# Kernel tuning notes

Measured on AMD Instinct MI355X. Metric: run time of the kernel, lower is better.

Reference implementation:

```python
import jax, jax.numpy as jnp
import numpy as np

B, T, D = 2, 2048, 1024
K, F = 8, 4096
LAMBDA = 0.5


def setup_inputs() -> dict:
    key = jax.random.key(0)
    ks = jax.random.split(key, 8)
    s = 0.02
    return {
        "x": jax.random.normal(ks[0], (B, T, D), dtype=jnp.float32),
        "prev_logits": jax.random.normal(ks[1], (B, T, K), dtype=jnp.float32),
        "Wt": jax.random.normal(ks[2], (D, K), dtype=jnp.float32) * s,
        "Wgt": jax.random.normal(ks[3], (K, K), dtype=jnp.float32) * s,
        "We_logits": jnp.zeros((K,), dtype=jnp.float32),
        "W1": jax.random.normal(ks[4], (K, D, F), dtype=jnp.float32) * s,
        "b1": jnp.zeros((K, F), dtype=jnp.float32),
        "W2": jax.random.normal(ks[5], (K, F, D), dtype=jnp.float32) * s,
        "b2": jnp.zeros((K, D), dtype=jnp.float32),
    }


def reference(x, prev_logits, Wt, Wgt, We_logits, W1, b1, W2, b2):
    # gating: softmax over router logits, sigmoid-threshold multi-hot mask
    logits = jnp.einsum("btd,dk->btk", x, Wt) + jnp.einsum("btk,kj->btj", prev_logits, Wgt)
    st = jax.nn.softmax(logits, axis=-1)                       # (B,T,K)
    We = jax.nn.sigmoid(We_logits)                             # (K,)
    mask = (st > LAMBDA * We).astype(x.dtype)                  # (B,T,K)
    g = st * mask
    sel_counts = mask.sum(axis=(0, 1))                         # (K,)
    avg_density = mask.sum(axis=-1).mean()                     # scalar

    # dense multi-expert FFN: every expert on every token (dropout=0 / eval)
    h = jax.nn.gelu(jnp.einsum("btd,kdf->bktf", x, W1) + b1[:, None, :], approximate=False)
    outk = jnp.einsum("bktf,kfd->bktd", h, W2) + b2[:, None, :]  # (B,K,T,D)
    y = jnp.einsum("btk,bktd->btd", g, outk)
    y = y / (g.sum(axis=-1, keepdims=True) + 1e-6)
    return y, jax.lax.stop_gradient(logits), sel_counts, avg_density
```

## Files before the change

kernel.cpp:

```cpp
#include <hip/hip_runtime.h>
#include <cstdint>
#include <cstddef>

#define NB 2
#define NTT 2048
#define ND 1024
#define NK 8
#define NF 4096
#define NTOK (NB*NTT)
#define LAMBDA_C 0.5f

#define Y_SZ   (NTOK*ND)
#define LG_OFF Y_SZ
#define SC_OFF (LG_OFF + NTOK*NK)
#define AD_OFF (SC_OFF + NK)

#define WS_CNT    0
#define WS_SEG    8
#define WS_NTILES 17
#define WS_TILEK  32
#define WS_TILER  1056
#define WS_PTOK   4096
#define WS_PCOEF  36864
#define WS_COEF   69632
#define WS_X16    102400
#define WS_H      2199552

#define BM 128
#define BN 128
#define BK 64
#define SPLITK2 4
#define KT 16

#define ASL0 0u
#define ASL1 16384u
#define BSL0 32768u
#define BSL1 49152u

typedef float  f32x4  __attribute__((ext_vector_type(4)));
typedef float  f32x16 __attribute__((ext_vector_type(16)));
typedef _Float16 f16x8 __attribute__((ext_vector_type(8)));
typedef unsigned int u32x4 __attribute__((ext_vector_type(4)));

__device__ __forceinline__ unsigned int pkrtz(float a, float b){
    auto h = __builtin_amdgcn_cvt_pkrtz(a, b);
    return __builtin_bit_cast(unsigned int, h);
}
__device__ __forceinline__ float gelu_exact(float v){
    return 0.5f * v * (1.0f + erff(v * 0.70710678118654752440f));
}

__global__ __launch_bounds__(256) void k_xcast(const float* __restrict__ x,
                                               unsigned short* __restrict__ x16)
{
    int i = (blockIdx.x*256 + threadIdx.x) * 16;
    const f32x4* src = (const f32x4*)(x + i);
    f32x4 v0 = src[0], v1 = src[1], v2 = src[2], v3 = src[3];
    u32x4 o0 = {pkrtz(v0[0],v0[1]), pkrtz(v0[2],v0[3]), pkrtz(v1[0],v1[1]), pkrtz(v1[2],v1[3])};
    u32x4 o1 = {pkrtz(v2[0],v2[1]), pkrtz(v2[2],v2[3]), pkrtz(v3[0],v3[1]), pkrtz(v3[2],v3[3])};
    *(u32x4*)(x16 + i)     = o0;
    *(u32x4*)(x16 + i + 8) = o1;
}

__global__ __launch_bounds__(256) void k_gating(
    const float* __restrict__ x, const float* __restrict__ pl,
    const float* __restrict__ Wt, const float* __restrict__ Wgt,
    const float* __restrict__ Wel, float* __restrict__ out,
    float* __restrict__ coef, int* __restrict__ cnt)
{
    int t = blockIdx.x;
    const float* xt = x + (size_t)t * ND;
    float acc[NK] = {0,0,0,0,0,0,0,0};
    for (int d = threadIdx.x; d < ND; d += 256){
        float xv = xt[d];
        const float4* w = (const float4*)(Wt + (size_t)d * NK);
        float4 w0 = w[0], w1 = w[1];
        acc[0] += xv*w0.x; acc[1] += xv*w0.y; acc[2] += xv*w0.z; acc[3] += xv*w0.w;
        acc[4] += xv*w1.x; acc[5] += xv*w1.y; acc[6] += xv*w1.z; acc[7] += xv*w1.w;
    }
    __shared__ float red[4][NK];
    #pragma unroll
    for (int k = 0; k < NK; k++){
        float v = acc[k];
        #pragma unroll
        for (int off = 32; off; off >>= 1) v += __shfl_down(v, off);
        if ((threadIdx.x & 63) == 0) red[threadIdx.x >> 6][k] = v;
    }
    __syncthreads();
    if (threadIdx.x == 0){
        const float* p = pl + (size_t)t * NK;
        float pv[NK];
        #pragma unroll
        for (int j = 0; j < NK; j++) pv[j] = p[j];
        float lg[NK]; float mx = -1e30f;
        #pragma unroll
        for (int k = 0; k < NK; k++){
            float v = red[0][k] + red[1][k] + red[2][k] + red[3][k];
            #pragma unroll
            for (int j = 0; j < NK; j++) v += pv[j] * Wgt[j*NK + k];
            lg[k] = v; mx = fmaxf(mx, v);
            out[LG_OFF + (size_t)t*NK + k] = v;
        }
        float e[NK]; float s = 0.f;
        #pragma unroll
        for (int k = 0; k < NK; k++){ e[k] = expf(lg[k] - mx); s += e[k]; }
        float g[NK]; float gsum = 0.f;
        #pragma unroll
        for (int k = 0; k < NK; k++){
            float st = e[k] / s;
            float we = 1.f / (1.f + expf(-Wel[k]));
            bool m = st > LAMBDA_C * we;
            g[k] = m ? st : 0.f;
            gsum += g[k];
        }
        float inv = 1.f / (gsum + 1e-6f);
        #pragma unroll
        for (int k = 0; k < NK; k++){
            coef[(size_t)t*NK + k] = g[k] * inv;
            if (g[k] > 0.f) atomicAdd(&cnt[k], 1);
        }
    }
}

__global__ __launch_bounds__(256) void k_scan(
    const float* __restrict__ coef, int* __restrict__ wsi,
    float* __restrict__ wsf, int pair_cap)
{
    int k = blockIdx.x;
    const int* cnt = wsi + WS_CNT;
    int base = 0;
    for (int j = 0; j < k; j++) base += cnt[j];
    int tid = threadIdx.x, lane = tid & 63, w = tid >> 6;
    __shared__ int wsum[4];
    __shared__ int sbase;
    if (tid == 0){
        sbase = base;
        wsi[WS_SEG + k] = base;
        if (k == NK-1) wsi[WS_SEG + NK] = base + cnt[k];
    }
    __syncthreads();
    int* ptok = wsi + WS_PTOK;
    float* pc = wsf + WS_PCOEF;
    for (int c0 = 0; c0 < NTOK; c0 += 256){
        int t = c0 + tid;
        float c = coef[(size_t)t*NK + k];
        bool m = c > 0.f;
        unsigned long long bal = __ballot(m);
        int pre = __popcll(bal & ((1ull << lane) - 1ull));
        if (lane == 0) wsum[w] = __popcll(bal);
        __syncthreads();
        int b = sbase;
        for (int j = 0; j < w; j++) b += wsum[j];
        if (m){
            int pos = b + pre;
            if (pos < pair_cap){ ptok[pos] = t; pc[pos] = c; }
        }
        __syncthreads();
        if (tid == 0) sbase += wsum[0] + wsum[1] + wsum[2] + wsum[3];
        __syncthreads();
    }
}

__global__ void k_tiles(int* __restrict__ wsi, float* __restrict__ out, int pair_cap)
{
    if (threadIdx.x == 0 && blockIdx.x == 0){
        const int* cnt = wsi + WS_CNT;
        const int* seg = wsi + WS_SEG;
        int total = 0;
        for (int k = 0; k < NK; k++){ total += cnt[k]; out[SC_OFF + k] = (float)cnt[k]; }
        out[AD_OFF] = (float)total / (float)NTOK;
        int nt = 0;
        for (int k = 0; k < NK; k++){
            int e = min(seg[k+1], pair_cap);
            for (int r = seg[k]; r < e; r += BM){
                wsi[WS_TILEK + nt] = k; wsi[WS_TILER + nt] = r; nt++;
            }
        }
        wsi[WS_NTILES] = nt;
    }
}

#define XCD_PART_LOOP(nwork)                                              \
    int q_ = (nwork) >> 3, rr_ = (nwork) & 7;                             \
    int xcd_ = blockIdx.x & 7;                                            \
    int slot_ = blockIdx.x >> 3;                                          \
    int nslot_ = gridDim.x >> 3;                                          \
    int cntw_ = q_ + (xcd_ < rr_ ? 1 : 0);                                \
    int start_ = xcd_ * q_ + (xcd_ < rr_ ? xcd_ : rr_);                   \
    for (int p_ = slot_; p_ < cntw_; p_ += nslot_)


#define LOADB(tt_, LDW_)                                                  \
  { const float* bn_ = bsrc + (size_t)((tt_)*BK + bu*8)*(LDW_);           \
    _Pragma("unroll")                                                     \
    for (int r9_ = 0; r9_ < 8; r9_++) gb[r9_] = *(const f32x4*)(bn_ + (size_t)r9_*(LDW_)); }

#define CVTWRB(BO_)                                                       \
  { _Pragma("unroll")                                                     \
    for (int j9_ = 0; j9_ < 4; j9_++){                                    \
        unsigned p0_ = pkrtz(gb[0][j9_], gb[1][j9_]);                     \
        unsigned p1_ = pkrtz(gb[2][j9_], gb[3][j9_]);                     \
        unsigned p2_ = pkrtz(gb[4][j9_], gb[5][j9_]);                     \
        unsigned p3_ = pkrtz(gb[6][j9_], gb[7][j9_]);                     \
        unsigned c9_ = (unsigned)(bg*4 + j9_);                            \
        unsigned off9_ = (BO_) + c9_*128u + (((unsigned)bu*16u) ^ (((c9_>>1)&7u)<<4)); \
        *(u32x4*)(&lds[off9_]) = (u32x4){p0_, p1_, p2_, p3_};             \
    } }

#define GLL_A(AO_, tt_)                                                   \
  { _Pragma("unroll")                                                     \
    for (int c9_ = 0; c9_ < 4; c9_++){                                    \
        const unsigned short* g9_ = asrc[c9_] + (tt_)*BK + asw8;          \
        __builtin_amdgcn_global_load_lds(                                 \
            (const __attribute__((address_space(1))) void*)g9_,           \
            (__attribute__((address_space(3))) void*)(&lds[(AO_) + (unsigned)((wv*4 + c9_)*1024)]), \
            16, 0, 0);                                                    \
    } }

#define MFMA_PH(AO_, BO_)                                                 \
  { __builtin_amdgcn_s_setprio(1);                                        \
    _Pragma("unroll")                                                     \
    for (int s9_ = 0; s9_ < 4; s9_++){                                    \
        unsigned ko_ = (unsigned)(s9_*32) + ah16;                         \
        f16x8 a0_ = *(const f16x8*)(&lds[(AO_) + arow0*128u + (ko_ ^ axr)]); \
        f16x8 a1_ = *(const f16x8*)(&lds[(AO_) + arow1*128u + (ko_ ^ axr)]); \
        f16x8 b0_ = *(const f16x8*)(&lds[(BO_) + bcol0*128u + (ko_ ^ bxr)]); \
        f16x8 b1_ = *(const f16x8*)(&lds[(BO_) + bcol1*128u + (ko_ ^ bxr)]); \
        acc00 = __builtin_amdgcn_mfma_f32_32x32x16_f16(a0_, b0_, acc00, 0,0,0); \
        acc01 = __builtin_amdgcn_mfma_f32_32x32x16_f16(a0_, b1_, acc01, 0,0,0); \
        acc10 = __builtin_amdgcn_mfma_f32_32x32x16_f16(a1_, b0_, acc10, 0,0,0); \
        acc11 = __builtin_amdgcn_mfma_f32_32x32x16_f16(a1_, b1_, acc11, 0,0,0); \
    }                                                                     \
    __builtin_amdgcn_s_setprio(0); }

#define PIPE_LOOP(LDW_)                                                   \
    f32x16 acc00 = {0}, acc01 = {0}, acc10 = {0}, acc11 = {0};            \
    LOADB(0, LDW_)                                                        \
    GLL_A(ASL0, 0)                                                        \
    for (int t = 0; t < KT-1; t++){                                       \
        if ((t & 1) == 0){                                                \
            CVTWRB(BSL0)                                                  \
            LOADB(t+1, LDW_)                                              \
            asm volatile("s_waitcnt vmcnt(8) lgkmcnt(0)" ::: "memory");   \
            __builtin_amdgcn_s_barrier();                                 \
            __builtin_amdgcn_sched_barrier(0);                            \
            GLL_A(ASL1, t+1)                                              \
            MFMA_PH(ASL0, BSL0)                                           \
        } else {                                                          \
            CVTWRB(BSL1)                                                  \
            LOADB(t+1, LDW_)                                              \
            asm volatile("s_waitcnt vmcnt(8) lgkmcnt(0)" ::: "memory");   \
            __builtin_amdgcn_s_barrier();                                 \
            __builtin_amdgcn_sched_barrier(0);                            \
            GLL_A(ASL0, t+1)                                              \
            MFMA_PH(ASL1, BSL1)                                           \
        }                                                                 \
    }                                                                     \
    {                                     \
        CVTWRB(BSL1)                                                      \
        asm volatile("s_waitcnt vmcnt(0) lgkmcnt(0)" ::: "memory");       \
        __builtin_amdgcn_s_barrier();                                     \
        __builtin_amdgcn_sched_barrier(0);                                \
        MFMA_PH(ASL1, BSL1)                                               \
    }

__global__ __launch_bounds__(256, 2) void k_gemm1(
    const unsigned short* __restrict__ x16, const float* __restrict__ W1,
    const float* __restrict__ b1, const int* __restrict__ wsi,
    unsigned short* __restrict__ hbuf, int pair_cap)
{
    __shared__ char lds[65536];
    __shared__ int stok[BM];
    const int* seg  = wsi + WS_SEG;
    const int* tk   = wsi + WS_TILEK;
    const int* tr   = wsi + WS_TILER;
    const int* ptok = wsi + WS_PTOK;
    int ntm = wsi[WS_NTILES];
    int nwork = ntm * (NF / BN);
    int tid  = threadIdx.x;
    int L    = tid & 63;
    int wv   = tid >> 6;
    int wr = wv >> 1, wc = wv & 1;
    int bu = tid >> 5, bg = tid & 31;
    unsigned l31 = (unsigned)(L & 31);
    unsigned arow0 = (unsigned)(wr*64) + l31;
    unsigned arow1 = arow0 + 32u;
    unsigned bcol0 = BSL0*0 + (unsigned)(wc*64) + l31;
    unsigned bcol1 = bcol0 + 32u;
    unsigned ah16 = (unsigned)((L >> 5) * 16);
    unsigned axr  = (unsigned)((L & 7) << 4);
    unsigned bxr  = ((l31 >> 1) & 7u) << 4;
    int asw8 = ((L & 7) ^ (L >> 3)) * 8;
    int srow = L >> 3;

    XCD_PART_LOOP(nwork){
        int widx = start_ + p_;
        int mt = widx % ntm;
        int ft = widx / ntm;
        int kexp = tk[mt];
        int row0 = tr[mt];
        int nrows = min(BM, seg[kexp+1] - row0);
        int f0 = ft * BN;
        __syncthreads();
        if (tid < BM){
            int r = row0 + tid;
            stok[tid] = (tid < nrows && r < pair_cap) ? ptok[r] : ptok[row0];
        }
        __syncthreads();
        const unsigned short* asrc[4];
        #pragma unroll
        for (int c = 0; c < 4; c++)
            asrc[c] = x16 + (size_t)stok[(wv*4 + c)*8 + srow] * ND;
        const float* bsrc = W1 + (size_t)kexp*ND*NF + f0 + bg*4;
        f32x4 gb[8];
        PIPE_LOOP(NF)
        const float* b1k = b1 + (size_t)kexp*NF;
        #pragma unroll
        for (int n = 0; n < 2; n++){
            int f = f0 + wc*64 + n*32 + (int)l31;
            float bv = b1k[f];
            #pragma unroll
            for (int m = 0; m < 2; m++){
                int rbase = wr*64 + m*32 + 4*(L>>5);
                const f32x16& a = (m==0) ? (n==0 ? acc00 : acc01) : (n==0 ? acc10 : acc11);
                #pragma unroll
                for (int rg = 0; rg < 16; rg++){
                    int row = rbase + (rg&3) + 8*(rg>>2);
                    if (row < nrows && row0 + row < pair_cap){
                        float v = gelu_exact(a[rg] + bv);
                        hbuf[(size_t)(row0+row)*NF + f] = (unsigned short)(pkrtz(v, 0.f) & 0xffffu);
                    }
                }
            }
        }
    }
}

__global__ __launch_bounds__(256, 2) void k_gemm2(
    const unsigned short* __restrict__ hbuf, const float* __restrict__ W2,
    const float* __restrict__ b2, const int* __restrict__ wsi,
    const float* __restrict__ wsf, float* __restrict__ out, int pair_cap)
{
    __shared__ char lds[65536];
    __shared__ int stok[BM];
    __shared__ float scoef[BM];
    const int* seg  = wsi + WS_SEG;
    const int* tk   = wsi + WS_TILEK;
    const int* tr   = wsi + WS_TILER;
    const int* ptok = wsi + WS_PTOK;
    const float* pcoef = wsf + WS_PCOEF;
    int ntm = wsi[WS_NTILES];
    int nwork = ntm * (ND / BN) * SPLITK2;
    int tid  = threadIdx.x;
    int L    = tid & 63;
    int wv   = tid >> 6;
    int wr = wv >> 1, wc = wv & 1;
    int bu = tid >> 5, bg = tid & 31;
    unsigned l31 = (unsigned)(L & 31);
    unsigned arow0 = (unsigned)(wr*64) + l31;
    unsigned arow1 = arow0 + 32u;
    unsigned bcol0 = (unsigned)(wc*64) + l31;
    unsigned bcol1 = bcol0 + 32u;
    unsigned ah16 = (unsigned)((L >> 5) * 16);
    unsigned axr  = (unsigned)((L & 7) << 4);
    unsigned bxr  = ((l31 >> 1) & 7u) << 4;
    int asw8 = ((L & 7) ^ (L >> 3)) * 8;
    int srow = L >> 3;

    XCD_PART_LOOP(nwork){
        int widx = start_ + p_;
        int mt = widx % ntm;
        int rest = widx / ntm;
        int dt = rest & 7;
        int spk = rest >> 3;
        int kexp = tk[mt];
        int row0 = tr[mt];
        int nrows = min(BM, seg[kexp+1] - row0);
        int d0 = dt * BN;
        __syncthreads();
        if (tid < BM){
            int r = row0 + tid;
            bool v = (tid < nrows && r < pair_cap);
            stok[tid]  = v ? ptok[r] : 0;
            scoef[tid] = v ? pcoef[r] : 0.f;
        }
        __syncthreads();
        const unsigned short* asrc[4];
        #pragma unroll
        for (int c = 0; c < 4; c++){
            int rg = row0 + (wv*4 + c)*8 + srow;
            if (rg >= pair_cap) rg = pair_cap - 1;
            asrc[c] = hbuf + (size_t)rg*NF + spk*(NF/SPLITK2);
        }
        const float* bsrc = W2 + (size_t)kexp*NF*ND + (size_t)spk*(NF/SPLITK2)*ND + d0 + bg*4;
        f32x4 gb[8];
        PIPE_LOOP(ND)
        const float* b2k = b2 + (size_t)kexp*ND;
        #pragma unroll
        for (int n = 0; n < 2; n++){
            int d = d0 + wc*64 + n*32 + (int)l31;
            float bv = (spk == 0) ? b2k[d] : 0.f;
            #pragma unroll
            for (int m = 0; m < 2; m++){
                int rbase = wr*64 + m*32 + 4*(L>>5);
                const f32x16& a = (m==0) ? (n==0 ? acc00 : acc01) : (n==0 ? acc10 : acc11);
                #pragma unroll
                for (int rg = 0; rg < 16; rg++){
                    int row = rbase + (rg&3) + 8*(rg>>2);
                    if (row < nrows && row0 + row < pair_cap){
                        float c = scoef[row];
                        atomicAdd(&out[(size_t)stok[row]*ND + d], c * (a[rg] + bv));
                    }
                }
            }
        }
    }
}

extern "C" void kernel_launch(void* const* d_in, const int* in_sizes, int n_in,
                              void* d_out, int out_size, void* d_ws, size_t ws_size,
                              hipStream_t stream)
{
    const float* x   = (const float*)d_in[0];
    const float* pl  = (const float*)d_in[1];
    const float* Wt  = (const float*)d_in[2];
    const float* Wgt = (const float*)d_in[3];
    const float* Wel = (const float*)d_in[4];
    const float* W1  = (const float*)d_in[5];
    const float* b1  = (const float*)d_in[6];
    const float* W2  = (const float*)d_in[7];
    const float* b2  = (const float*)d_in[8];
    float* out = (float*)d_out;
    int* wsi   = (int*)d_ws;
    float* wsf = (float*)d_ws;
    unsigned short* x16  = (unsigned short*)((char*)d_ws + (size_t)WS_X16*4);
    unsigned short* hbuf = (unsigned short*)((char*)d_ws + (size_t)WS_H*4);

    long long avail = (long long)ws_size - (long long)WS_H*4;
    long long cap = avail / ((long long)NF*2);
    if (cap > (long long)NTOK*NK) cap = (long long)NTOK*NK;
    if (cap < 0) cap = 0;
    int pair_cap = (int)cap;

    hipMemsetAsync(d_out, 0, (size_t)out_size*sizeof(float), stream);
    hipMemsetAsync(d_ws, 0, 32, stream);
    k_xcast<<<1024, 256, 0, stream>>>(x, x16);
    k_gating<<<NTOK, 256, 0, stream>>>(x, pl, Wt, Wgt, Wel, out, wsf + WS_COEF, wsi + WS_CNT);
    if (pair_cap > 0){
        k_scan<<<NK, 256, 0, stream>>>(wsf + WS_COEF, wsi, wsf, pair_cap);
        k_tiles<<<1, 64, 0, stream>>>(wsi, out, pair_cap);
        k_gemm1<<<2048, 256, 0, stream>>>(x16, W1, b1, wsi, hbuf, pair_cap);
        k_gemm2<<<2048, 256, 0, stream>>>(hbuf, W2, b2, wsi, wsf, out, pair_cap);
    }
}
```

Baseline: 262.5 us.

## Double-buffer fp32 weight register loads and remap thread-to-B-tile layout with new swizzle

```diff
diff --git a/kernel.cpp b/kernel.cpp
--- a/kernel.cpp
+++ b/kernel.cpp
@@ -190,20 +190,20 @@
     for (int p_ = slot_; p_ < cntw_; p_ += nslot_)
 
 
-#define LOADB(tt_, LDW_)                                                  \
+#define LOADB(G_, tt_, LDW_)                                              \
   { const float* bn_ = bsrc + (size_t)((tt_)*BK + bu*8)*(LDW_);           \
     _Pragma("unroll")                                                     \
-    for (int r9_ = 0; r9_ < 8; r9_++) gb[r9_] = *(const f32x4*)(bn_ + (size_t)r9_*(LDW_)); }
-
-#define CVTWRB(BO_)                                                       \
+    for (int r9_ = 0; r9_ < 8; r9_++) G_[r9_] = *(const f32x4*)(bn_ + (size_t)r9_*(LDW_)); }
+
+#define CVTWRB(G_, BO_)                                                   \
   { _Pragma("unroll")                                                     \
     for (int j9_ = 0; j9_ < 4; j9_++){                                    \
-        unsigned p0_ = pkrtz(gb[0][j9_], gb[1][j9_]);                     \
-        unsigned p1_ = pkrtz(gb[2][j9_], gb[3][j9_]);                     \
-        unsigned p2_ = pkrtz(gb[4][j9_], gb[5][j9_]);                     \
-        unsigned p3_ = pkrtz(gb[6][j9_], gb[7][j9_]);                     \
+        unsigned p0_ = pkrtz(G_[0][j9_], G_[1][j9_]);                     \
+        unsigned p1_ = pkrtz(G_[2][j9_], G_[3][j9_]);                     \
+        unsigned p2_ = pkrtz(G_[4][j9_], G_[5][j9_]);                     \
+        unsigned p3_ = pkrtz(G_[6][j9_], G_[7][j9_]);                     \
         unsigned c9_ = (unsigned)(bg*4 + j9_);                            \
-        unsigned off9_ = (BO_) + c9_*128u + (((unsigned)bu*16u) ^ (((c9_>>1)&7u)<<4)); \
+        unsigned off9_ = (BO_) + c9_*128u + (((unsigned)bu*16u) ^ (((c9_>>2)&7u)<<4)); \
         *(u32x4*)(&lds[off9_]) = (u32x4){p0_, p1_, p2_, p3_};             \
     } }
 
@@ -233,36 +233,33 @@
     }                                                                     \
     __builtin_amdgcn_s_setprio(0); }
 
+#define PIPE_BODY(G_, AS_, BS_, AN_, tt_, LDW_)                           \
+    asm volatile("s_waitcnt vmcnt(12)" ::: "memory");                     \
+    CVTWRB(G_, BS_)                                                       \
+    asm volatile("s_waitcnt vmcnt(8) lgkmcnt(0)" ::: "memory");           \
+    __builtin_amdgcn_s_barrier();                                         \
+    __builtin_amdgcn_sched_barrier(0);                                    \
+    GLL_A(AN_, (tt_)+1)                                                   \
+    if ((tt_) + 2 < KT){ LOADB(G_, (tt_)+2, LDW_) }                       \
+    MFMA_PH(AS_, BS_)
+
 #define PIPE_LOOP(LDW_)                                                   \
     f32x16 acc00 = {0}, acc01 = {0}, acc10 = {0}, acc11 = {0};            \
-    LOADB(0, LDW_)                                                        \
+    f32x4 genA[8], genB[8];                                               \
+    LOADB(genA, 0, LDW_)                                                  \
+    LOADB(genB, 1, LDW_)                                                  \
     GLL_A(ASL0, 0)                                                        \
     for (int t = 0; t < KT-1; t++){                                       \
-        if ((t & 1) == 0){                                                \
-            CVTWRB(BSL0)                                                  \
-            LOADB(t+1, LDW_)                                              \
-            asm volatile("s_waitcnt vmcnt(8) lgkmcnt(0)" ::: "memory");   \
-            __builtin_amdgcn_s_barrier();                                 \
-            __builtin_amdgcn_sched_barrier(0);                            \
-            GLL_A(ASL1, t+1)                                              \
-            MFMA_PH(ASL0, BSL0)                                           \
-        } else {                                                          \
-            CVTWRB(BSL1)                                                  \
-            LOADB(t+1, LDW_)                                              \
-            asm volatile("s_waitcnt vmcnt(8) lgkmcnt(0)" ::: "memory");   \
-            __builtin_amdgcn_s_barrier();                                 \
-            __builtin_amdgcn_sched_barrier(0);                            \
-            GLL_A(ASL0, t+1)                                              \
-            MFMA_PH(ASL1, BSL1)                                           \
-        }                                                                 \
+        if ((t & 1) == 0){ PIPE_BODY(genA, ASL0, BSL0, ASL1, t, LDW_) }   \
+        else             { PIPE_BODY(genB, ASL1, BSL1, ASL0, t, LDW_) }   \
     }                                                                     \
-    {                                     \
-        CVTWRB(BSL1)                                                      \
-        asm volatile("s_waitcnt vmcnt(0) lgkmcnt(0)" ::: "memory");       \
-        __builtin_amdgcn_s_barrier();                                     \
-        __builtin_amdgcn_sched_barrier(0);                                \
-        MFMA_PH(ASL1, BSL1)                                               \
-    }
+                \
+    asm volatile("s_waitcnt vmcnt(4)" ::: "memory");                      \
+    CVTWRB(genB, BSL1)                                                    \
+    asm volatile("s_waitcnt vmcnt(0) lgkmcnt(0)" ::: "memory");           \
+    __builtin_amdgcn_s_barrier();                                         \
+    __builtin_amdgcn_sched_barrier(0);                                    \
+    MFMA_PH(ASL1, BSL1)
 
 __global__ __launch_bounds__(256, 2) void k_gemm1(
     const unsigned short* __restrict__ x16, const float* __restrict__ W1,
@@ -281,15 +278,15 @@
     int L    = tid & 63;
     int wv   = tid >> 6;
     int wr = wv >> 1, wc = wv & 1;
-    int bu = tid >> 5, bg = tid & 31;
+    int bu = tid & 7, bg = tid >> 3;
     unsigned l31 = (unsigned)(L & 31);
     unsigned arow0 = (unsigned)(wr*64) + l31;
     unsigned arow1 = arow0 + 32u;
-    unsigned bcol0 = BSL0*0 + (unsigned)(wc*64) + l31;
+    unsigned bcol0 = (unsigned)(wc*64) + l31;
     unsigned bcol1 = bcol0 + 32u;
     unsigned ah16 = (unsigned)((L >> 5) * 16);
     unsigned axr  = (unsigned)((L & 7) << 4);
-    unsigned bxr  = ((l31 >> 1) & 7u) << 4;
+    unsigned bxr  = ((l31 >> 2) & 7u) << 4;
     int asw8 = ((L & 7) ^ (L >> 3)) * 8;
     int srow = L >> 3;
 
@@ -312,7 +309,6 @@
         for (int c = 0; c < 4; c++)
             asrc[c] = x16 + (size_t)stok[(wv*4 + c)*8 + srow] * ND;
         const float* bsrc = W1 + (size_t)kexp*ND*NF + f0 + bg*4;
-        f32x4 gb[8];
         PIPE_LOOP(NF)
         const float* b1k = b1 + (size_t)kexp*NF;
         #pragma unroll
@@ -355,7 +351,7 @@
     int L    = tid & 63;
     int wv   = tid >> 6;
     int wr = wv >> 1, wc = wv & 1;
-    int bu = tid >> 5, bg = tid & 31;
+    int bu = tid & 7, bg = tid >> 3;
     unsigned l31 = (unsigned)(L & 31);
     unsigned arow0 = (unsigned)(wr*64) + l31;
     unsigned arow1 = arow0 + 32u;
@@ -363,7 +359,7 @@
     unsigned bcol1 = bcol0 + 32u;
     unsigned ah16 = (unsigned)((L >> 5) * 16);
     unsigned axr  = (unsigned)((L & 7) << 4);
-    unsigned bxr  = ((l31 >> 1) & 7u) << 4;
+    unsigned bxr  = ((l31 >> 2) & 7u) << 4;
     int asw8 = ((L & 7) ^ (L >> 3)) * 8;
     int srow = L >> 3;
 
@@ -393,7 +389,6 @@
             asrc[c] = hbuf + (size_t)rg*NF + spk*(NF/SPLITK2);
         }
         const float* bsrc = W2 + (size_t)kexp*NF*ND + (size_t)spk*(NF/SPLITK2)*ND + d0 + bg*4;
-        f32x4 gb[8];
         PIPE_LOOP(ND)
         const float* b2k = b2 + (size_t)kexp*ND;
         #pragma unroll
```

Result: slower. 599.5 us (+128.4%).
